# Kernel optimization log

Measured on AMD Instinct MI355X. Metric: run time of the kernel, lower is better.

## Reference

```python
import jax, jax.numpy as jnp
import numpy as np

D_MODEL = 1024
D_HIDDEN = 4096
BATCH = 4
SEQ = 2048
EPS = 1e-5
SLOPE = 0.01  # LeakyReLU default negative_slope


def layer_norm(x, g, b):
    m = jnp.mean(x, axis=-1, keepdims=True)
    v = jnp.mean(jnp.square(x - m), axis=-1, keepdims=True)
    return (x - m) * jax.lax.rsqrt(v + EPS) * g + b


def leaky_relu(x):
    return jnp.where(x >= 0, x, SLOPE * x)


def setup_inputs() -> dict:
    key = jax.random.key(0)
    ks = jax.random.split(key, 8)
    scale = D_MODEL ** 0.5
    x = jax.random.normal(ks[0], (BATCH, SEQ, D_MODEL), dtype=jnp.float32)
    qk = jax.random.normal(ks[1], (D_MODEL, D_MODEL), dtype=jnp.float32) / scale
    ov = jax.random.normal(ks[2], (D_MODEL, D_MODEL), dtype=jnp.float32) / scale
    ln1_g = jnp.ones((D_MODEL,), jnp.float32)
    ln1_b = jnp.zeros((D_MODEL,), jnp.float32)
    ln2_g = jnp.ones((D_MODEL,), jnp.float32)
    ln2_b = jnp.zeros((D_MODEL,), jnp.float32)
    # nn.Linear default init: uniform(-1/sqrt(fan_in), 1/sqrt(fan_in))
    def lin(k, fan_in, fan_out):
        k1, k2 = jax.random.split(k)
        bd = 1.0 / np.sqrt(fan_in)
        W = jax.random.uniform(k1, (fan_out, fan_in), jnp.float32, -bd, bd)
        b = jax.random.uniform(k2, (fan_out,), jnp.float32, -bd, bd)
        return W, b
    W_up, b_up = lin(ks[3], D_MODEL, D_HIDDEN)
    W_h, b_h = lin(ks[4], D_HIDDEN, D_HIDDEN)
    W_down, b_down = lin(ks[5], D_HIDDEN, D_MODEL)
    return {"x": x, "qk": qk, "ov": ov, "ln1_g": ln1_g, "ln1_b": ln1_b,
            "ln2_g": ln2_g, "ln2_b": ln2_b, "W_up": W_up, "b_up": b_up,
            "W_h": W_h, "b_h": b_h, "W_down": W_down, "b_down": b_down}


def reference(x, qk, ov, ln1_g, ln1_b, ln2_g, ln2_b,
              W_up, b_up, W_h, b_h, W_down, b_down):
    scale = D_MODEL ** 0.5
    # --- attention on ln1(x) ---
    h = layer_norm(x, ln1_g, ln1_b)                     # [B,S,D]
    scores = jnp.einsum('bsd,de,bte->bst', h, qk, h) / scale  # [B,S,S]
    n = h.shape[1]
    causal = jnp.tril(jnp.ones((n, n), bool))
    scores = jnp.where(causal, scores, -jnp.inf)
    probs = jax.nn.softmax(scores, axis=-1)
    attn = jnp.einsum('bst,btd,de->bse', probs, h, ov)  # [B,S,D]
    x = x + attn
    # --- MLP on ln2(x) ---
    h2 = layer_norm(x, ln2_g, ln2_b)
    a = leaky_relu(h2 @ W_up.T + b_up)
    a = leaky_relu(a @ W_h.T + b_h)
    a = leaky_relu(a @ W_down.T + b_down)
    return x + a
```

## Files before the change

kernel.cpp:

```cpp
#include <hip/hip_runtime.h>
#include <stdint.h>


typedef __attribute__((ext_vector_type(4))) float  f32x4;
typedef __attribute__((ext_vector_type(8))) __bf16 bf16v8;
typedef __attribute__((ext_vector_type(8))) unsigned short u16x8;
typedef unsigned short ushort_t;
typedef unsigned int   u32;

#define SLOPE 0.01f

__device__ __forceinline__ ushort_t f2bf(float f) {
  u32 u = __builtin_bit_cast(u32, f);
  u32 r = (u + 0x7FFFu + ((u >> 16) & 1u)) >> 16;
  return (ushort_t)r;
}
__device__ __forceinline__ float bf2f(ushort_t b) {
  u32 u = ((u32)b) << 16;
  return __builtin_bit_cast(float, u);
}

__device__ __forceinline__ void gload_lds16(const void* g, void* l) {
  __builtin_amdgcn_global_load_lds(
      (const __attribute__((address_space(1))) u32*)g,
      (__attribute__((address_space(3))) u32*)l, 16, 0, 0);
}

template<int EPI>
__global__ __launch_bounds__(512, 1)
void gemm_nt8(const ushort_t* __restrict__ A, const ushort_t* __restrict__ B,
              void* __restrict__ Cv, const float* __restrict__ bias,
              int M, int N, int K)
{
  extern __shared__ char smem[];
  const ushort_t* lds = (const ushort_t*)smem;
  const int tid = threadIdx.x;
  const int l   = tid & 63;
  const int nwg = gridDim.x * gridDim.y;
  const int orig = blockIdx.y * gridDim.x + blockIdx.x;
  const int q8 = nwg >> 3, r8 = nwg & 7;
  const int xcd = orig & 7, io = orig >> 3;
  const int logical = (xcd < r8 ? xcd * (q8 + 1) : r8 * (q8 + 1) + (xcd - r8) * q8) + io;
  const int m0 = (logical / gridDim.x) * 256;
  const int n0 = (logical % gridDim.x) * 256;
  const int wid = tid >> 6;
  const int wm = (wid >> 2) * 128;
  const int wn = (wid & 3) * 64;
  const int nt = K >> 5;

  const int  sg      = (((tid & 3) ^ ((tid >> 3) & 3))) * 8;
  const long rowA0   = (long)(m0 +       (tid >> 2)) * K;
  const long rowA1   = (long)(m0 + 128 + (tid >> 2)) * K;
  const long rowB0   = (long)(n0 +       (tid >> 2)) * K;
  const long rowB1   = (long)(n0 + 128 + (tid >> 2)) * K;
  const int  wbase16 = (tid & ~63) * 16;

#define STAGE(TT) do {                                                        \
    const long _k  = (long)(TT) * 32;                                         \
    char* _ra = (char*)smem + ((TT) & 3) * 32768 + wbase16;                   \
    char* _rb = _ra + 16384;                                                  \
    gload_lds16(A + rowA0 + _k + sg, _ra);                                    \
    gload_lds16(A + rowA1 + _k + sg, _ra + 8192);                             \
    gload_lds16(B + rowB0 + _k + sg, _rb);                                    \
    gload_lds16(B + rowB1 + _k + sg, _rb + 8192);                             \
  } while (0)

  const int fr  = l & 15;
  const int fsl = (((l >> 4) ^ ((l >> 1) & 3))) * 8;

  f32x4 acc[8][4] = {};

  STAGE(0);
  if (nt > 1) STAGE(1);
  if (nt > 2) STAGE(2);
  if (nt > 2)      { asm volatile("s_waitcnt vmcnt(8)" ::: "memory"); }
  else if (nt > 1) { asm volatile("s_waitcnt vmcnt(4)" ::: "memory"); }
  else             { asm volatile("s_waitcnt vmcnt(0)" ::: "memory"); }
  __builtin_amdgcn_s_barrier();
  __builtin_amdgcn_sched_barrier(0);

  for (int t = 0; t < nt; ++t) {
    const int buf = t & 3;
    const ushort_t* rA = lds + buf * 16384 +        (wm + fr) * 32 + fsl;
    const ushort_t* rB = lds + buf * 16384 + 8192 + (wn + fr) * 32 + fsl;
    bf16v8 av[8], bv[4];
#pragma unroll
    for (int mf = 0; mf < 8; mf++) av[mf] = *(const bf16v8*)(rA + mf * 512);
#pragma unroll
    for (int nf = 0; nf < 4; nf++) bv[nf] = *(const bf16v8*)(rB + nf * 512);

    if (t + 3 < nt) STAGE(t + 3);

    __builtin_amdgcn_s_setprio(1);
#pragma unroll
    for (int mf = 0; mf < 8; mf++)
#pragma unroll
      for (int nf = 0; nf < 4; nf++)
        acc[mf][nf] = __builtin_amdgcn_mfma_f32_16x16x32_bf16(
            av[mf], bv[nf], acc[mf][nf], 0, 0, 0);
    __builtin_amdgcn_s_setprio(0);

    if (t <= nt - 4) {
      asm volatile("s_waitcnt vmcnt(8)" ::: "memory");
      __builtin_amdgcn_s_barrier();
      __builtin_amdgcn_sched_barrier(0);
    } else if (t == nt - 3) {
      asm volatile("s_waitcnt vmcnt(4)" ::: "memory");
      __builtin_amdgcn_s_barrier();
      __builtin_amdgcn_sched_barrier(0);
    } else if (t == nt - 2) {
      asm volatile("s_waitcnt vmcnt(0)" ::: "memory");
      __builtin_amdgcn_s_barrier();
      __builtin_amdgcn_sched_barrier(0);
    }
  }
#undef STAGE

  const int lr = (l >> 4) * 4;
#pragma unroll
  for (int mf = 0; mf < 8; mf++) {
    const int row0 = m0 + wm + mf * 16 + lr;
#pragma unroll
    for (int nf = 0; nf < 4; nf++) {
      const int col = n0 + wn + nf * 16 + fr;
      const float bcol = bias ? bias[col] : 0.f;
#pragma unroll
      for (int r = 0; r < 4; r++) {
        float v = acc[mf][nf][r];
        if constexpr (EPI == 2) {
          v += bcol;
          v = v >= 0.f ? v : SLOPE * v;
          ((ushort_t*)Cv)[(long)(row0 + r) * N + col] = f2bf(v);
        } else {
          ((ushort_t*)Cv)[(long)(row0 + r) * N + col] = f2bf(v);
        }
      }
    }
  }
}

template<int EPI>
__global__ __launch_bounds__(512, 1)
void gemm_nt8b(const ushort_t* __restrict__ A, const ushort_t* __restrict__ B,
               void* __restrict__ Cv, const float* __restrict__ bias,
               const float* __restrict__ resid,
               int M, int N, int K)
{
  extern __shared__ char smem[];
  const ushort_t* lds = (const ushort_t*)smem;
  const int tid = threadIdx.x;
  const int l   = tid & 63;
  const int nwg = gridDim.x * gridDim.y;
  const int orig = blockIdx.y * gridDim.x + blockIdx.x;
  const int q8 = nwg >> 3, r8 = nwg & 7;
  const int xcd = orig & 7, io = orig >> 3;
  const int logical = (xcd < r8 ? xcd * (q8 + 1) : r8 * (q8 + 1) + (xcd - r8) * q8) + io;
  const int m0 = (logical / gridDim.x) * 256;
  const int n0 = (logical % gridDim.x) * 128;
  const int wid = tid >> 6;
  const int wm = (wid >> 1) * 64;
  const int wn = (wid & 1) * 64;
  const int nt = K >> 5;

  const int  sg      = (((tid & 3) ^ ((tid >> 3) & 3))) * 8;
  const long rowA0   = (long)(m0 +       (tid >> 2)) * K;
  const long rowA1   = (long)(m0 + 128 + (tid >> 2)) * K;
  const long rowB0   = (long)(n0 +       (tid >> 2)) * K;
  const int  wbase16 = (tid & ~63) * 16;

#define STAGEB(TT) do {                                                       \
    const long _k  = (long)(TT) * 32;                                         \
    char* _ra = (char*)smem + ((TT) & 3) * 24576 + wbase16;                   \
    char* _rb = _ra + 16384;                                                  \
    gload_lds16(A + rowA0 + _k + sg, _ra);                                    \
    gload_lds16(A + rowA1 + _k + sg, _ra + 8192);                             \
    gload_lds16(B + rowB0 + _k + sg, _rb);                                    \
  } while (0)

  const int fr  = l & 15;
  const int fsl = (((l >> 4) ^ ((l >> 1) & 3))) * 8;

  f32x4 acc[4][4] = {};

  STAGEB(0);
  if (nt > 1) STAGEB(1);
  if (nt > 2) STAGEB(2);
  if (nt > 2)      { asm volatile("s_waitcnt vmcnt(6)" ::: "memory"); }
  else if (nt > 1) { asm volatile("s_waitcnt vmcnt(3)" ::: "memory"); }
  else             { asm volatile("s_waitcnt vmcnt(0)" ::: "memory"); }
  __builtin_amdgcn_s_barrier();
  __builtin_amdgcn_sched_barrier(0);

  for (int t = 0; t < nt; ++t) {
    const int buf = t & 3;
    const ushort_t* rA = lds + buf * 12288 +        (wm + fr) * 32 + fsl;
    const ushort_t* rB = lds + buf * 12288 + 8192 + (wn + fr) * 32 + fsl;
    bf16v8 av[4], bv[4];
#pragma unroll
    for (int mf = 0; mf < 4; mf++) av[mf] = *(const bf16v8*)(rA + mf * 512);
#pragma unroll
    for (int nf = 0; nf < 4; nf++) bv[nf] = *(const bf16v8*)(rB + nf * 512);

    if (t + 3 < nt) STAGEB(t + 3);

    __builtin_amdgcn_s_setprio(1);
#pragma unroll
    for (int mf = 0; mf < 4; mf++)
#pragma unroll
      for (int nf = 0; nf < 4; nf++)
        acc[mf][nf] = __builtin_amdgcn_mfma_f32_16x16x32_bf16(
            av[mf], bv[nf], acc[mf][nf], 0, 0, 0);
    __builtin_amdgcn_s_setprio(0);

    if (t <= nt - 4) {
      asm volatile("s_waitcnt vmcnt(6)" ::: "memory");
      __builtin_amdgcn_s_barrier();
      __builtin_amdgcn_sched_barrier(0);
    } else if (t == nt - 3) {
      asm volatile("s_waitcnt vmcnt(3)" ::: "memory");
      __builtin_amdgcn_s_barrier();
      __builtin_amdgcn_sched_barrier(0);
    } else if (t == nt - 2) {
      asm volatile("s_waitcnt vmcnt(0)" ::: "memory");
      __builtin_amdgcn_s_barrier();
      __builtin_amdgcn_sched_barrier(0);
    }
  }
#undef STAGEB

  const int lr = (l >> 4) * 4;
#pragma unroll
  for (int mf = 0; mf < 4; mf++) {
    const int row0 = m0 + wm + mf * 16 + lr;
#pragma unroll
    for (int nf = 0; nf < 4; nf++) {
      const int col = n0 + wn + nf * 16 + fr;
      const float bcol = (EPI == 4 && bias) ? bias[col] : 0.f;
#pragma unroll
      for (int r = 0; r < 4; r++) {
        float v = acc[mf][nf][r];
        const long idx = (long)(row0 + r) * N + col;
        if constexpr (EPI == 0) {
          ((ushort_t*)Cv)[idx] = f2bf(v);
        } else if constexpr (EPI == 3) {
          ((float*)Cv)[idx] = v + resid[idx];
        } else {
          v += bcol;
          v = v >= 0.f ? v : SLOPE * v;
          ((float*)Cv)[idx] = v + resid[idx];
        }
      }
    }
  }
}

template<int EPI, bool CAUSAL, bool KLIM>
__global__ __launch_bounds__(256)
void gemm_nt(const ushort_t* __restrict__ A, const ushort_t* __restrict__ B,
             void* __restrict__ Cv, const float* __restrict__ bias,
             const float* __restrict__ resid,
             int M, int N, int K, long sAb, long sBb, long sCb)
{
  __shared__ ushort_t lA[128 * 32];
  __shared__ ushort_t lB[128 * 32];
  const int tid = threadIdx.x;
  const int w = tid >> 6;
  const int l = tid & 63;
  const int nwg = gridDim.x * gridDim.y;
  const int orig = blockIdx.y * gridDim.x + blockIdx.x;
  const int q8 = nwg >> 3, r8 = nwg & 7;
  const int xcd = orig & 7, io = orig >> 3;
  const int logical = (xcd < r8 ? xcd * (q8 + 1) : r8 * (q8 + 1) + (xcd - r8) * q8) + io;
  const int m0 = (logical / gridDim.x) * 128;
  const int n0 = (logical % gridDim.x) * 128;
  if (CAUSAL && n0 > m0 + 127) return;
  const long bz = blockIdx.z;
  A += bz * sAb;
  B += bz * sBb;
  int Keff = K;
  if (KLIM) Keff = min(K, m0 + 128);

  const ushort_t* gA = A + (long)(m0 + w * 32 + (l >> 2)) * K + (l & 3) * 8;
  const ushort_t* gB = B + (long)(n0 + w * 32 + (l >> 2)) * K + (l & 3) * 8;
  ushort_t* lAw0 = &lA[(w * 32) * 32];
  ushort_t* lAw1 = &lA[(w * 32 + 16) * 32];
  ushort_t* lBw0 = &lB[(w * 32) * 32];
  ushort_t* lBw1 = &lB[(w * 32 + 16) * 32];
  const int wm = (w >> 1) * 64, wn = (w & 1) * 64;

  f32x4 acc[4][4] = {};

  for (int k0 = 0; k0 < Keff; k0 += 32) {
    gload_lds16(gA,                 lAw0);
    gload_lds16(gA + (long)16 * K,  lAw1);
    gload_lds16(gB,                 lBw0);
    gload_lds16(gB + (long)16 * K,  lBw1);
    gA += 32; gB += 32;
    __syncthreads();

    bf16v8 af[4], bfr[4];
#pragma unroll
    for (int m = 0; m < 4; m++)
      af[m] = *(const bf16v8*)&lA[(wm + m * 16 + (l & 15)) * 32 + (l >> 4) * 8];
#pragma unroll
    for (int n = 0; n < 4; n++)
      bfr[n] = *(const bf16v8*)&lB[(wn + n * 16 + (l & 15)) * 32 + (l >> 4) * 8];
#pragma unroll
    for (int m = 0; m < 4; m++)
#pragma unroll
      for (int n = 0; n < 4; n++)
        acc[m][n] = __builtin_amdgcn_mfma_f32_16x16x32_bf16(af[m], bfr[n], acc[m][n], 0, 0, 0);
    __syncthreads();
  }

  const int lr = (l >> 4) * 4;
  const int lc = l & 15;
#pragma unroll
  for (int m = 0; m < 4; m++) {
    const int row0 = m0 + wm + m * 16 + lr;
#pragma unroll
    for (int n = 0; n < 4; n++) {
      const int col = n0 + wn + n * 16 + lc;
#pragma unroll
      for (int r = 0; r < 4; r++) {
        float v = acc[m][n][r];
        const long idx = bz * sCb + (long)(row0 + r) * N + col;
        if constexpr (EPI == 0) {
          ((ushort_t*)Cv)[idx] = f2bf(v);
        } else if constexpr (EPI == 2) {
          v += bias[col];
          v = v >= 0.f ? v : SLOPE * v;
          ((ushort_t*)Cv)[idx] = f2bf(v);
        } else if constexpr (EPI == 3) {
          ((float*)Cv)[idx] = v + resid[idx];
        } else {
          v += bias[col];
          v = v >= 0.f ? v : SLOPE * v;
          ((float*)Cv)[idx] = v + resid[idx];
        }
      }
    }
  }
}

__global__ __launch_bounds__(256)
void ln_kernel(const float* __restrict__ x, const float* __restrict__ g,
               const float* __restrict__ bta, ushort_t* __restrict__ o)
{
  const long row = blockIdx.x;
  const int tid = threadIdx.x;
  const float4 v = *((const float4*)(x + row * 1024) + tid);
  float s  = v.x + v.y + v.z + v.w;
  float ss = v.x * v.x + v.y * v.y + v.z * v.z + v.w * v.w;
  for (int o2 = 32; o2 > 0; o2 >>= 1) {
    s  += __shfl_down(s, o2);
    ss += __shfl_down(ss, o2);
  }
  __shared__ float rs[4], rss[4];
  const int w = tid >> 6, l = tid & 63;
  if (l == 0) { rs[w] = s; rss[w] = ss; }
  __syncthreads();
  if (tid == 0) {
    float a = 0, c = 0;
    for (int i = 0; i < 4; i++) { a += rs[i]; c += rss[i]; }
    rs[0] = a; rss[0] = c;
  }
  __syncthreads();
  const float mean = rs[0] * (1.f / 1024.f);
  const float var  = rss[0] * (1.f / 1024.f) - mean * mean;
  const float rstd = rsqrtf(var + 1e-5f);
  const int c0 = tid * 4;
  ushort_t* orow = o + row * 1024;
  const float* vp = (const float*)&v;
#pragma unroll
  for (int i = 0; i < 4; i++)
    orow[c0 + i] = f2bf((vp[i] - mean) * rstd * g[c0 + i] + bta[c0 + i]);
}

__global__ __launch_bounds__(256)
void softmax_kernel(ushort_t* __restrict__ sc)
{
  const long row = blockIdx.x;
  const int s = (int)(row & 2047);
  const int tid = threadIdx.x;
  ushort_t* srow = sc + row * 2048;
  const int t0 = tid * 8;
  u16x8 raw = *(const u16x8*)(srow + t0);
  float v[8];
  const float rsc = 1.0f / 32.0f;
  float mx = -3e38f;
#pragma unroll
  for (int i = 0; i < 8; i++) {
    float f = bf2f(raw[i]) * rsc;
    v[i] = (t0 + i <= s) ? f : -3e38f;
    mx = fmaxf(mx, v[i]);
  }
  for (int o = 32; o > 0; o >>= 1) mx = fmaxf(mx, __shfl_down(mx, o));
  __shared__ float red[8];
  const int w = tid >> 6, l = tid & 63;
  if (l == 0) red[w] = mx;
  __syncthreads();
  if (tid == 0) {
    float m2 = red[0];
    for (int i = 1; i < 4; i++) m2 = fmaxf(m2, red[i]);
    red[0] = m2;
  }
  __syncthreads();
  const float m = red[0];
  float sum = 0.f;
#pragma unroll
  for (int i = 0; i < 8; i++) {
    float e = (t0 + i <= s) ? __expf(v[i] - m) : 0.f;
    v[i] = e; sum += e;
  }
  for (int o = 32; o > 0; o >>= 1) sum += __shfl_down(sum, o);
  if (l == 0) red[4 + w] = sum;
  __syncthreads();
  if (tid == 0) {
    float s2 = 0;
    for (int i = 0; i < 4; i++) s2 += red[4 + i];
    red[0] = 1.0f / s2;
  }
  __syncthreads();
  const float inv = red[0];
#pragma unroll
  for (int i = 0; i < 8; i++) srow[t0 + i] = f2bf(v[i] * inv);
}

__global__ __launch_bounds__(256)
void cast3_bf16(const float* __restrict__ a, const float* __restrict__ b,
                const float* __restrict__ c, ushort_t* __restrict__ oa,
                ushort_t* __restrict__ ob, ushort_t* __restrict__ oc)
{
  long i = ((long)blockIdx.x * 256 + threadIdx.x) * 4;
  const float* src; ushort_t* dst;
  if (i < 4194304L)        { src = a; dst = oa; }
  else if (i < 8388608L)   { src = b + (0 - 4194304L); dst = ob - 4194304L; }
  else                     { src = c + (0 - 8388608L); dst = oc - 8388608L; }
  float4 v = *(const float4*)(src + i);
  dst[i]     = f2bf(v.x);
  dst[i + 1] = f2bf(v.y);
  dst[i + 2] = f2bf(v.z);
  dst[i + 3] = f2bf(v.w);
}

__global__ __launch_bounds__(256)
void transpose_cast2(const float* __restrict__ s0, ushort_t* __restrict__ d0,
                     const float* __restrict__ s1, ushort_t* __restrict__ d1)
{
  __shared__ ushort_t t[32][33];
  const float* in = blockIdx.z ? s1 : s0;
  ushort_t*    o  = blockIdx.z ? d1 : d0;
  const int tx = threadIdx.x & 31, ty = threadIdx.x >> 5;
  const int r0 = blockIdx.y * 32, c0 = blockIdx.x * 32;
#pragma unroll
  for (int i = 0; i < 4; i++)
    t[ty + i * 8][tx] = f2bf(in[(long)(r0 + ty + i * 8) * 1024 + c0 + tx]);
  __syncthreads();
#pragma unroll
  for (int i = 0; i < 4; i++)
    o[(long)(c0 + ty + i * 8) * 1024 + r0 + tx] = t[tx][ty + i * 8];
}

__global__ __launch_bounds__(256)
void transpose_bf16(const ushort_t* __restrict__ in, ushort_t* __restrict__ o,
                    int R, int C)
{
  __shared__ ushort_t t[32][33];
  const long bz = blockIdx.z;
  in += bz * (long)R * C;
  o  += bz * (long)R * C;
  const int tx = threadIdx.x & 31, ty = threadIdx.x >> 5;
  const int r0 = blockIdx.y * 32, c0 = blockIdx.x * 32;
#pragma unroll
  for (int i = 0; i < 4; i++)
    t[ty + i * 8][tx] = in[(long)(r0 + ty + i * 8) * C + c0 + tx];
  __syncthreads();
#pragma unroll
  for (int i = 0; i < 4; i++)
    o[(long)(c0 + ty + i * 8) * R + r0 + tx] = t[tx][ty + i * 8];
}

extern "C" void kernel_launch(void* const* d_in, const int* in_sizes, int n_in,
                              void* d_out, int out_size, void* d_ws, size_t ws_size,
                              hipStream_t stream)
{
  const float* x      = (const float*)d_in[0];
  const float* qk     = (const float*)d_in[1];
  const float* ov     = (const float*)d_in[2];
  const float* ln1_g  = (const float*)d_in[3];
  const float* ln1_b  = (const float*)d_in[4];
  const float* ln2_g  = (const float*)d_in[5];
  const float* ln2_b  = (const float*)d_in[6];
  const float* W_up   = (const float*)d_in[7];
  const float* b_up   = (const float*)d_in[8];
  const float* W_h    = (const float*)d_in[9];
  const float* b_h    = (const float*)d_in[10];
  const float* W_down = (const float*)d_in[11];
  const float* b_down = (const float*)d_in[12];
  float* out = (float*)d_out;
  char* ws = (char*)d_ws;
  const long MB = 1024L * 1024L;

  ushort_t* wqT    = (ushort_t*)(ws +   0 * MB);
  ushort_t* woT    = (ushort_t*)(ws +   2 * MB);
  ushort_t* h      = (ushort_t*)(ws +   4 * MB);
  ushort_t* hT     = (ushort_t*)(ws +  20 * MB);
  ushort_t* q      = (ushort_t*)(ws +  36 * MB);
  ushort_t* scores = (ushort_t*)(ws +  52 * MB);
  ushort_t* h2     = h;
  ushort_t* attnh  = q;
  ushort_t* wu     = hT;
  ushort_t* wd     = (ushort_t*)(ws +  28 * MB);
  ushort_t* wh     = q;
  ushort_t* a1     = (ushort_t*)(ws +  68 * MB);
  ushort_t* a2c    = (ushort_t*)(ws + 100 * MB);
  ushort_t* a2f    = (ushort_t*)(ws + 132 * MB);

  const bool ws197 = ws_size >= (size_t)(197 * MB);
  const bool ws166 = ws_size >= (size_t)(166 * MB);

  transpose_cast2<<<dim3(32, 32, 2), 256, 0, stream>>>(qk, wqT, ov, woT);
  ln_kernel<<<8192, 256, 0, stream>>>(x, ln1_g, ln1_b, h);
  transpose_bf16<<<dim3(32, 64, 4), 256, 0, stream>>>(h, hT, 2048, 1024);

  gemm_nt8b<0><<<dim3(8, 32, 1), 512, 98304, stream>>>(
      h, wqT, q, nullptr, nullptr, 8192, 1024, 1024);
  gemm_nt<0, true, false><<<dim3(16, 16, 4), 256, 0, stream>>>(
      q, h, scores, nullptr, nullptr, 2048, 2048, 1024,
      2048L * 1024, 2048L * 1024, 2048L * 2048);
  softmax_kernel<<<8192, 256, 0, stream>>>(scores);
  gemm_nt<0, false, true><<<dim3(8, 16, 4), 256, 0, stream>>>(
      scores, hT, attnh, nullptr, nullptr, 2048, 1024, 2048,
      2048L * 2048, 1024L * 2048, 2048L * 1024);
  gemm_nt8b<3><<<dim3(8, 32, 1), 512, 98304, stream>>>(
      attnh, woT, out, nullptr, x, 8192, 1024, 1024);

  ln_kernel<<<8192, 256, 0, stream>>>(out, ln2_g, ln2_b, h2);
  cast3_bf16<<<24576, 256, 0, stream>>>(W_up, W_down, W_h, wu, wd, wh);

  if (ws197) {
    gemm_nt8<2><<<dim3(16, 32, 1), 512, 131072, stream>>>(
        h2, wu, a1, b_up, 8192, 4096, 1024);
    gemm_nt8<2><<<dim3(16, 32, 1), 512, 131072, stream>>>(
        a1, wh, a2f, b_h, 8192, 4096, 4096);
    gemm_nt8b<4><<<dim3(8, 32, 1), 512, 98304, stream>>>(
        a2f, wd, out, b_down, out, 8192, 1024, 4096);
  } else if (ws166) {
    for (int c = 0; c < 2; c++) {
      const long r0 = (long)c * 4096;
      gemm_nt8<2><<<dim3(16, 16, 1), 512, 131072, stream>>>(
          h2 + r0 * 1024, wu, a1, b_up, 4096, 4096, 1024);
      gemm_nt8<2><<<dim3(16, 16, 1), 512, 131072, stream>>>(
          a1, wh, a2c + r0 * 4096, b_h, 4096, 4096, 4096);
    }
    gemm_nt<4, false, false><<<dim3(8, 64, 1), 256, 0, stream>>>(
        a2c, wd, out, b_down, out, 8192, 1024, 4096, 0, 0, 0);
  } else {
    for (int c = 0; c < 2; c++) {
      const long r0 = (long)c * 4096;
      gemm_nt8<2><<<dim3(16, 16, 1), 512, 131072, stream>>>(
          h2 + r0 * 1024, wu, a1, b_up, 4096, 4096, 1024);
      gemm_nt8<2><<<dim3(16, 16, 1), 512, 131072, stream>>>(
          a1, wh, a2c, b_h, 4096, 4096, 4096);
      gemm_nt<4, false, false><<<dim3(8, 32, 1), 256, 0, stream>>>(
          a2c, wd, out + r0 * 1024, b_down, out + r0 * 1024, 4096, 1024, 4096, 0, 0, 0);
    }
  }
}
```

Before: 632.3 us.

## Run attention score and PV GEMMs on the large-tile pipelined GEMM kernels

Adds batch strides to both large-tile GEMM kernels, plus a causal tile-skip option to the 256x256 kernel and a causal K-limit option to the 256x128 kernel. The QK^T score GEMM and the probs x hT GEMM now use these 512-thread, LDS-pipelined kernels instead of the generic 256-thread gemm_nt. The goal is to give the attention matmuls the same tiling and data reuse as the MLP GEMMs. The risk is poor load balance: with the coarser grid, many blocks exit early or stop at a short K, leaving fewer blocks to cover the 256 CUs.

```diff
diff --git a/kernel.cpp b/kernel.cpp
--- a/kernel.cpp
+++ b/kernel.cpp
@@ -26,11 +26,11 @@
       (__attribute__((address_space(3))) u32*)l, 16, 0, 0);
 }
 
-template<int EPI>
+template<int EPI, bool CAUSAL>
 __global__ __launch_bounds__(512, 1)
 void gemm_nt8(const ushort_t* __restrict__ A, const ushort_t* __restrict__ B,
               void* __restrict__ Cv, const float* __restrict__ bias,
-              int M, int N, int K)
+              int M, int N, int K, long sAb, long sBb, long sCb)
 {
   extern __shared__ char smem[];
   const ushort_t* lds = (const ushort_t*)smem;
@@ -43,6 +43,10 @@
   const int logical = (xcd < r8 ? xcd * (q8 + 1) : r8 * (q8 + 1) + (xcd - r8) * q8) + io;
   const int m0 = (logical / gridDim.x) * 256;
   const int n0 = (logical % gridDim.x) * 256;
+  if (CAUSAL && n0 > m0 + 255) return;
+  A += (long)blockIdx.z * sAb;
+  B += (long)blockIdx.z * sBb;
+  const long coff = (long)blockIdx.z * sCb;
   const int wid = tid >> 6;
   const int wm = (wid >> 2) * 128;
   const int wn = (wid & 3) * 64;
@@ -123,28 +127,28 @@
 #pragma unroll
     for (int nf = 0; nf < 4; nf++) {
       const int col = n0 + wn + nf * 16 + fr;
-      const float bcol = bias ? bias[col] : 0.f;
+      const float bcol = (EPI == 2) ? bias[col] : 0.f;
 #pragma unroll
       for (int r = 0; r < 4; r++) {
         float v = acc[mf][nf][r];
         if constexpr (EPI == 2) {
           v += bcol;
           v = v >= 0.f ? v : SLOPE * v;
-          ((ushort_t*)Cv)[(long)(row0 + r) * N + col] = f2bf(v);
+          ((ushort_t*)Cv)[coff + (long)(row0 + r) * N + col] = f2bf(v);
         } else {
-          ((ushort_t*)Cv)[(long)(row0 + r) * N + col] = f2bf(v);
+          ((ushort_t*)Cv)[coff + (long)(row0 + r) * N + col] = f2bf(v);
         }
       }
     }
   }
 }
 
-template<int EPI>
+template<int EPI, bool KLIM>
 __global__ __launch_bounds__(512, 1)
 void gemm_nt8b(const ushort_t* __restrict__ A, const ushort_t* __restrict__ B,
                void* __restrict__ Cv, const float* __restrict__ bias,
                const float* __restrict__ resid,
-               int M, int N, int K)
+               int M, int N, int K, long sAb, long sBb, long sCb)
 {
   extern __shared__ char smem[];
   const ushort_t* lds = (const ushort_t*)smem;
@@ -157,10 +161,15 @@
   const int logical = (xcd < r8 ? xcd * (q8 + 1) : r8 * (q8 + 1) + (xcd - r8) * q8) + io;
   const int m0 = (logical / gridDim.x) * 256;
   const int n0 = (logical % gridDim.x) * 128;
+  A += (long)blockIdx.z * sAb;
+  B += (long)blockIdx.z * sBb;
+  const long coff = (long)blockIdx.z * sCb;
   const int wid = tid >> 6;
   const int wm = (wid >> 1) * 64;
   const int wn = (wid & 1) * 64;
-  const int nt = K >> 5;
+  int Keff = K;
+  if (KLIM) Keff = min(K, m0 + 256);
+  const int nt = Keff >> 5;
 
   const int  sg      = (((tid & 3) ^ ((tid >> 3) & 3))) * 8;
   const long rowA0   = (long)(m0 +       (tid >> 2)) * K;
@@ -235,11 +244,11 @@
 #pragma unroll
     for (int nf = 0; nf < 4; nf++) {
       const int col = n0 + wn + nf * 16 + fr;
-      const float bcol = (EPI == 4 && bias) ? bias[col] : 0.f;
+      const float bcol = (EPI == 4) ? bias[col] : 0.f;
 #pragma unroll
       for (int r = 0; r < 4; r++) {
         float v = acc[mf][nf][r];
-        const long idx = (long)(row0 + r) * N + col;
+        const long idx = coff + (long)(row0 + r) * N + col;
         if constexpr (EPI == 0) {
           ((ushort_t*)Cv)[idx] = f2bf(v);
         } else if constexpr (EPI == 3) {
@@ -524,45 +533,45 @@
   ln_kernel<<<8192, 256, 0, stream>>>(x, ln1_g, ln1_b, h);
   transpose_bf16<<<dim3(32, 64, 4), 256, 0, stream>>>(h, hT, 2048, 1024);
 
-  gemm_nt8b<0><<<dim3(8, 32, 1), 512, 98304, stream>>>(
-      h, wqT, q, nullptr, nullptr, 8192, 1024, 1024);
-  gemm_nt<0, true, false><<<dim3(16, 16, 4), 256, 0, stream>>>(
-      q, h, scores, nullptr, nullptr, 2048, 2048, 1024,
+  gemm_nt8b<0, false><<<dim3(8, 32, 1), 512, 98304, stream>>>(
+      h, wqT, q, nullptr, nullptr, 8192, 1024, 1024, 0, 0, 0);
+  gemm_nt8<0, true><<<dim3(8, 8, 4), 512, 131072, stream>>>(
+      q, h, scores, nullptr, 2048, 2048, 1024,
       2048L * 1024, 2048L * 1024, 2048L * 2048);
   softmax_kernel<<<8192, 256, 0, stream>>>(scores);
-  gemm_nt<0, false, true><<<dim3(8, 16, 4), 256, 0, stream>>>(
+  gemm_nt8b<0, true><<<dim3(8, 8, 4), 512, 98304, stream>>>(
       scores, hT, attnh, nullptr, nullptr, 2048, 1024, 2048,
       2048L * 2048, 1024L * 2048, 2048L * 1024);
-  gemm_nt8b<3><<<dim3(8, 32, 1), 512, 98304, stream>>>(
-      attnh, woT, out, nullptr, x, 8192, 1024, 1024);
+  gemm_nt8b<3, false><<<dim3(8, 32, 1), 512, 98304, stream>>>(
+      attnh, woT, out, nullptr, x, 8192, 1024, 1024, 0, 0, 0);
 
   ln_kernel<<<8192, 256, 0, stream>>>(out, ln2_g, ln2_b, h2);
   cast3_bf16<<<24576, 256, 0, stream>>>(W_up, W_down, W_h, wu, wd, wh);
 
   if (ws197) {
-    gemm_nt8<2><<<dim3(16, 32, 1), 512, 131072, stream>>>(
-        h2, wu, a1, b_up, 8192, 4096, 1024);
-    gemm_nt8<2><<<dim3(16, 32, 1), 512, 131072, stream>>>(
-        a1, wh, a2f, b_h, 8192, 4096, 4096);
-    gemm_nt8b<4><<<dim3(8, 32, 1), 512, 98304, stream>>>(
-        a2f, wd, out, b_down, out, 8192, 1024, 4096);
+    gemm_nt8<2, false><<<dim3(16, 32, 1), 512, 131072, stream>>>(
+        h2, wu, a1, b_up, 8192, 4096, 1024, 0, 0, 0);
+    gemm_nt8<2, false><<<dim3(16, 32, 1), 512, 131072, stream>>>(
+        a1, wh, a2f, b_h, 8192, 4096, 4096, 0, 0, 0);
+    gemm_nt8b<4, false><<<dim3(8, 32, 1), 512, 98304, stream>>>(
+        a2f, wd, out, b_down, out, 8192, 1024, 4096, 0, 0, 0);
   } else if (ws166) {
     for (int c = 0; c < 2; c++) {
       const long r0 = (long)c * 4096;
-      gemm_nt8<2><<<dim3(16, 16, 1), 512, 131072, stream>>>(
-          h2 + r0 * 1024, wu, a1, b_up, 4096, 4096, 1024);
-      gemm_nt8<2><<<dim3(16, 16, 1), 512, 131072, stream>>>(
-          a1, wh, a2c + r0 * 4096, b_h, 4096, 4096, 4096);
+      gemm_nt8<2, false><<<dim3(16, 16, 1), 512, 131072, stream>>>(
+          h2 + r0 * 1024, wu, a1, b_up, 4096, 4096, 1024, 0, 0, 0);
+      gemm_nt8<2, false><<<dim3(16, 16, 1), 512, 131072, stream>>>(
+          a1, wh, a2c + r0 * 4096, b_h, 4096, 4096, 4096, 0, 0, 0);
     }
     gemm_nt<4, false, false><<<dim3(8, 64, 1), 256, 0, stream>>>(
         a2c, wd, out, b_down, out, 8192, 1024, 4096, 0, 0, 0);
   } else {
     for (int c = 0; c < 2; c++) {
       const long r0 = (long)c * 4096;
-      gemm_nt8<2><<<dim3(16, 16, 1), 512, 131072, stream>>>(
-          h2 + r0 * 1024, wu, a1, b_up, 4096, 4096, 1024);
-      gemm_nt8<2><<<dim3(16, 16, 1), 512, 131072, stream>>>(
-          a1, wh, a2c, b_h, 4096, 4096, 4096);
+      gemm_nt8<2, false><<<dim3(16, 16, 1), 512, 131072, stream>>>(
+          h2 + r0 * 1024, wu, a1, b_up, 4096, 4096, 1024, 0, 0, 0);
+      gemm_nt8<2, false><<<dim3(16, 16, 1), 512, 131072, stream>>>(
+          a1, wh, a2c, b_h, 4096, 4096, 4096, 0, 0, 0);
       gemm_nt<4, false, false><<<dim3(8, 32, 1), 256, 0, stream>>>(
           a2c, wd, out + r0 * 1024, b_down, out + r0 * 1024, 4096, 1024, 4096, 0, 0, 0);
     }
```

After: 578.6 us (median of 2 runs). 8.5% less time.
